# Performance work log

Hardware: AMD Instinct MI355X
Metric: run time of the kernel (lower is better)

Reference implementation:

```python
import jax, jax.numpy as jnp
import numpy as np

B, T, D = 2, 2048, 2048
N_HEADS, N_KV, HEAD_DIM = 16, 8, 128
SOFTCAP = 50.0
BIG_NEG = -2.3819763e38
ROPE_BASE = 10000.0


def apply_rope(x, positions):
    # x: [B, L, N, H], positions: [B, L]
    H = x.shape[-1]
    half = H // 2
    fraction = 2.0 * jnp.arange(half, dtype=jnp.float32) / H
    timescale = ROPE_BASE ** fraction  # [H/2]
    sinusoid = positions.astype(jnp.float32)[:, :, None, None] / timescale[None, None, None, :]  # [B,L,1,H/2]
    sin, cos = jnp.sin(sinusoid), jnp.cos(sinusoid)
    first, second = jnp.split(x, 2, axis=-1)
    out = jnp.concatenate([first * cos - second * sin, second * cos + first * sin], axis=-1)
    return out.astype(x.dtype)


def setup_inputs() -> dict:
    key = jax.random.key(0)
    k1, k2, k3, k4 = jax.random.split(key, 4)
    x = jax.random.normal(k1, (B, T, D), dtype=jnp.float32)
    positions = jnp.broadcast_to(jnp.arange(T, dtype=jnp.int32), (B, T))
    # causal mask [B, 1, T, S]
    attn_mask = jnp.broadcast_to(jnp.tril(jnp.ones((T, T), dtype=bool))[None, None], (B, 1, T, T))
    s = 1.0 / np.sqrt(D)
    w_q = jax.random.normal(k2, (N_HEADS, D, HEAD_DIM), dtype=jnp.float32) * s
    w_kv = jax.random.normal(k3, (2, N_KV, D, HEAD_DIM), dtype=jnp.float32) * s
    w_out = jax.random.normal(k4, (N_HEADS, HEAD_DIM, D), dtype=jnp.float32) * (1.0 / np.sqrt(N_HEADS * HEAD_DIM))
    return {"x": x, "positions": positions, "attn_mask": attn_mask, "w_q": w_q, "w_kv": w_kv, "w_out": w_out}


def reference(x, positions, attn_mask, w_q, w_kv, w_out):
    # projections (GQA branch: num_kv_heads != num_heads)
    q = jnp.einsum('btd,ndh->btnh', x, w_q)            # [B,T,N,H]
    kv = jnp.einsum('bsd,cndh->cbsnh', x, w_kv)        # [2,B,S,K,H]
    k, v = kv[0], kv[1]
    q = apply_rope(q, positions) * (HEAD_DIM ** -0.5)  # rsqrt_head_dim
    k = apply_rope(k, positions)
    G = N_HEADS // N_KV
    q = q.reshape(B, T, N_KV, G, HEAD_DIM)             # B T K G H
    logits = jnp.einsum('btkgh,bskh->bkgts', q, k).astype(jnp.float32)
    logits = jnp.tanh(logits / SOFTCAP) * SOFTCAP
    masked = jnp.where(attn_mask[:, :, None, :, :], logits, BIG_NEG)
    probs = jax.nn.softmax(masked, axis=-1).astype(k.dtype)
    encoded = jnp.einsum('bkgts,bskh->btkgh', probs, v).reshape(B, T, N_HEADS, HEAD_DIM)
    return jnp.einsum('btnh,nhd->btd', encoded, w_out)
```

## Files before the change

kernel.cpp:

```cpp
#include <hip/hip_runtime.h>


typedef unsigned short u16;
typedef __attribute__((ext_vector_type(8))) short short8;
typedef __attribute__((ext_vector_type(4))) float floatx4;

static __device__ __forceinline__ u16 f2b(float f){
  unsigned u = __float_as_uint(f);
  u = (u + 0x7fffu + ((u >> 16) & 1u)) >> 16;
  return (u16)u;
}
static __device__ __forceinline__ float b2f(u16 u){
  return __uint_as_float(((unsigned)u) << 16);
}
static __device__ __forceinline__ void gload16(const u16* g, u16* l){
  __builtin_amdgcn_global_load_lds(
      (const __attribute__((address_space(1))) unsigned int*)g,
      (__attribute__((address_space(3))) unsigned int*)l, 16, 0, 0);
}

static __device__ void tr64(const float* __restrict__ s, u16* __restrict__ d,
                            int sRS, int dRS, float (*t)[65], int tid){
  #pragma unroll
  for(int i = 0; i < 16; i++){
    int idx = tid + 256 * i;
    t[idx >> 6][idx & 63] = s[(long)(idx >> 6) * sRS + (idx & 63)];
  }
  __syncthreads();
  #pragma unroll
  for(int i = 0; i < 16; i++){
    int idx = tid + 256 * i;
    d[(long)(idx >> 6) * dRS + (idx & 63)] = f2b(t[idx & 63][idx >> 6]);
  }
}

__global__ __launch_bounds__(256) void k_prep(
    const float* __restrict__ x, u16* __restrict__ xb,
    const float* __restrict__ wq, u16* __restrict__ wq_t,
    const float* __restrict__ wkv, u16* __restrict__ wkv_t,
    const float* __restrict__ wo, u16* __restrict__ wo_t,
    const int* __restrict__ pos, float* __restrict__ tab){
  __shared__ float t[64][65];
  int blk = blockIdx.x, tid = threadIdx.x;
  if(blk < 8192){
    int i = blk * 256 + tid;
    float4 v = ((const float4*)x)[i];
    ushort4 o = make_ushort4(f2b(v.x), f2b(v.y), f2b(v.z), f2b(v.w));
    ((ushort4*)xb)[i] = o;
  } else if(blk < 9216){
    int q = blk - 8192;
    int bx = q & 1, by = (q >> 1) & 31, bz = q >> 6;
    tr64(wq + (long)bz * 262144 + (long)by * 64 * 128 + bx * 64,
         wq_t + (long)bz * 262144 + (long)bx * 64 * 2048 + by * 64, 128, 2048, t, tid);
  } else if(blk < 10240){
    int q = blk - 9216;
    int bx = q & 1, by = (q >> 1) & 31, bz = q >> 6;
    tr64(wkv + (long)bz * 262144 + (long)by * 64 * 128 + bx * 64,
         wkv_t + (long)bz * 262144 + (long)bx * 64 * 2048 + by * 64, 128, 2048, t, tid);
  } else if(blk < 11264){
    int q = blk - 10240;
    int bx = q & 31, by = q >> 5;
    tr64(wo + (long)by * 64 * 2048 + bx * 64,
         wo_t + (long)bx * 64 * 2048 + by * 64, 2048, 2048, t, tid);
  } else {
    int idx = (blk - 11264) * 256 + tid;
    int row = idx >> 6, h = idx & 63;
    float pf = (float)pos[row];
    float inv = exp2f(-0.20762050593045077f * (float)h);
    float ang = pf * inv;
    tab[(row << 7) + h]      = sinf(ang);
    tab[(row << 7) + 64 + h] = cosf(ang);
  }
}

#define STAGE_A(tt, h) do{ \
  const u16* s_ = Ag + (tt) * 64 + (h) * 262144; \
  u16* d_ = ld + ss * 8192; \
  gload16(s_, d_); gload16(s_ + 131072, d_ + 4096); \
  ss++; if(ss == 10) ss = 0; }while(0)
#define STAGE_B(tt, h) do{ \
  const u16* s_ = Bg + (tt) * 64 + (h) * 262144; \
  u16* d_ = ld + ss * 8192; \
  gload16(s_, d_); gload16(s_ + 131072, d_ + 4096); \
  ss++; if(ss == 10) ss = 0; }while(0)

__global__ __launch_bounds__(512, 2) void k_gemm_qkv(
    const u16* __restrict__ A, const u16* __restrict__ wq_t, const u16* __restrict__ wkv_t,
    const float* __restrict__ tab,
    u16* __restrict__ qb, u16* __restrict__ kb, u16* __restrict__ vtp){
  __shared__ __attribute__((aligned(16))) u16 ring[81920];
  int mt = blockIdx.x, nt = blockIdx.y;
  const u16* Bt = (nt < 8) ? (wq_t + (long)nt * 524288)
                           : (wkv_t + (long)(nt - 8) * 524288);
  int tid = threadIdx.x;
  int lane = tid & 63, wave = tid >> 6, l15 = lane & 15, quad = lane >> 4;
  int wr = wave >> 2, wc = wave & 3;
  int cq0 = quad ^ (l15 & 7), cq1 = cq0 ^ 4;
  int srow = tid >> 3;
  int gch  = (tid & 7) ^ (srow & 7);
  const u16* Ag = A  + ((long)mt * 256 + srow) * 2048 + (gch << 3);
  const u16* Bg = Bt + (long)srow * 2048 + (gch << 3);
  u16* ld = ring + tid * 8;
  int aB = l15 << 6;
  int bB = ((wc & 1) * 64 + l15) << 6;
  int sa = wr;
  int sb = 2 + (wc >> 1);
  int ss = 0;
  floatx4 acc[8][4];
  const floatx4 fz = {0.f, 0.f, 0.f, 0.f};
  #pragma unroll
  for(int m = 0; m < 8; m++)
    #pragma unroll
    for(int n = 0; n < 4; n++) acc[m][n] = fz;

  STAGE_A(0, 0); STAGE_A(0, 1); STAGE_B(0, 0); STAGE_B(0, 1);
  STAGE_A(1, 0); STAGE_A(1, 1);
  asm volatile("s_waitcnt vmcnt(4)" ::: "memory");
  __builtin_amdgcn_s_barrier();

  #pragma unroll 1
  for(int t = 0; t < 32; t++){
    const u16* aS = ring + sa * 8192;
    const u16* bS = ring + sb * 8192;
    int tB = (t < 31) ? t + 1 : 31;
    int tA = (t < 30) ? t + 2 : 31;
    short8 a0[4], a1[4], b0[2], b1[2];
    #pragma unroll
    for(int n = 0; n < 2; n++){
      b0[n] = *(const short8*)(bS + bB + (n << 10) + (cq0 << 3));
      b1[n] = *(const short8*)(bS + bB + (n << 10) + (cq1 << 3));
    }
    #pragma unroll
    for(int m = 0; m < 4; m++){
      a0[m] = *(const short8*)(aS + aB + (m << 10) + (cq0 << 3));
      a1[m] = *(const short8*)(aS + aB + (m << 10) + (cq1 << 3));
    }
    STAGE_B(tB, 0);
    __builtin_amdgcn_s_barrier();
    asm volatile("s_waitcnt lgkmcnt(0)");
    __builtin_amdgcn_s_setprio(1);
    #pragma unroll
    for(int m = 0; m < 4; m++)
      #pragma unroll
      for(int n = 0; n < 2; n++)
        acc[m][n] = __builtin_amdgcn_mfma_f32_16x16x32_bf16(a0[m], b0[n], acc[m][n], 0, 0, 0);
    #pragma unroll
    for(int m = 0; m < 4; m++)
      #pragma unroll
      for(int n = 0; n < 2; n++)
        acc[m][n] = __builtin_amdgcn_mfma_f32_16x16x32_bf16(a1[m], b1[n], acc[m][n], 0, 0, 0);
    __builtin_amdgcn_s_setprio(0);
    __builtin_amdgcn_s_barrier();
    #pragma unroll
    for(int m = 0; m < 4; m++){
      a0[m] = *(const short8*)(aS + aB + 4096 + (m << 10) + (cq0 << 3));
      a1[m] = *(const short8*)(aS + aB + 4096 + (m << 10) + (cq1 << 3));
    }
    STAGE_B(tB, 1);
    __builtin_amdgcn_s_barrier();
    asm volatile("s_waitcnt lgkmcnt(0)");
    __builtin_amdgcn_s_setprio(1);
    #pragma unroll
    for(int m = 0; m < 4; m++)
      #pragma unroll
      for(int n = 0; n < 2; n++)
        acc[4 + m][n] = __builtin_amdgcn_mfma_f32_16x16x32_bf16(a0[m], b0[n], acc[4 + m][n], 0, 0, 0);
    #pragma unroll
    for(int m = 0; m < 4; m++)
      #pragma unroll
      for(int n = 0; n < 2; n++)
        acc[4 + m][n] = __builtin_amdgcn_mfma_f32_16x16x32_bf16(a1[m], b1[n], acc[4 + m][n], 0, 0, 0);
    __builtin_amdgcn_s_setprio(0);
    __builtin_amdgcn_s_barrier();
    #pragma unroll
    for(int n = 0; n < 2; n++){
      b0[n] = *(const short8*)(bS + bB + ((2 + n) << 10) + (cq0 << 3));
      b1[n] = *(const short8*)(bS + bB + ((2 + n) << 10) + (cq1 << 3));
    }
    STAGE_A(tA, 0);
    __builtin_amdgcn_s_barrier();
    asm volatile("s_waitcnt lgkmcnt(0)");
    __builtin_amdgcn_s_setprio(1);
    #pragma unroll
    for(int m = 0; m < 4; m++)
      #pragma unroll
      for(int n = 0; n < 2; n++)
        acc[4 + m][2 + n] = __builtin_amdgcn_mfma_f32_16x16x32_bf16(a0[m], b0[n], acc[4 + m][2 + n], 0, 0, 0);
    #pragma unroll
    for(int m = 0; m < 4; m++)
      #pragma unroll
      for(int n = 0; n < 2; n++)
        acc[4 + m][2 + n] = __builtin_amdgcn_mfma_f32_16x16x32_bf16(a1[m], b1[n], acc[4 + m][2 + n], 0, 0, 0);
    __builtin_amdgcn_s_setprio(0);
    __builtin_amdgcn_s_barrier();
    #pragma unroll
    for(int m = 0; m < 4; m++){
      a0[m] = *(const short8*)(aS + aB + (m << 10) + (cq0 << 3));
      a1[m] = *(const short8*)(aS + aB + (m << 10) + (cq1 << 3));
    }
    STAGE_A(tA, 1);
    asm volatile("s_waitcnt vmcnt(4)" ::: "memory");
    __builtin_amdgcn_s_barrier();
    asm volatile("s_waitcnt lgkmcnt(0)");
    __builtin_amdgcn_s_setprio(1);
    #pragma unroll
    for(int m = 0; m < 4; m++)
      #pragma unroll
      for(int n = 0; n < 2; n++)
        acc[m][2 + n] = __builtin_amdgcn_mfma_f32_16x16x32_bf16(a0[m], b0[n], acc[m][2 + n], 0, 0, 0);
    #pragma unroll
    for(int m = 0; m < 4; m++)
      #pragma unroll
      for(int n = 0; n < 2; n++)
        acc[m][2 + n] = __builtin_amdgcn_mfma_f32_16x16x32_bf16(a1[m], b1[n], acc[m][2 + n], 0, 0, 0);
    __builtin_amdgcn_s_setprio(0);
    __builtin_amdgcn_s_barrier();
    sa += 4; if(sa >= 10) sa -= 10;
    sb += 4; if(sb >= 10) sb -= 10;
  }

  asm volatile("s_waitcnt vmcnt(0)" ::: "memory");
  __syncthreads();
  u16* sT = ring;
  int grow0 = mt * 256;
  int hb = wc >> 1, wcl = wc & 1;
  #pragma unroll 1
  for(int hh = 0; hh < 2; hh++){
    if(hb == hh){
      #pragma unroll
      for(int m = 0; m < 8; m++){
        int row = wr * 128 + m * 16 + quad * 4;
        #pragma unroll
        for(int n = 0; n < 4; n++){
          int colh = wcl * 64 + n * 16 + l15;
          #pragma unroll
          for(int j = 0; j < 4; j++)
            sT[(row + j) * 132 + colh] = f2b(acc[m][n][j]);
        }
      }
    }
    __syncthreads();
    if(nt < 12){
      float scale = (nt < 8) ? 0.08838834764831845f : 1.0f;
      u16* dst = (nt < 8) ? qb : kb;
      int dS   = (nt < 8) ? 2048 : 1024;
      int dcol = (nt < 8) ? (nt * 2 + hh) * 128 : ((nt - 8) * 2 + hh) * 128;
      #pragma unroll
      for(int it = 0; it < 16; it++){
        int idx = tid + 512 * it;
        int row = idx >> 5, cw = idx & 31;
        int grow = grow0 + row;
        unsigned lo = *(const unsigned*)&sT[row * 132 + 2 * cw];
        unsigned hi = *(const unsigned*)&sT[row * 132 + 64 + 2 * cw];
        float2 sn = *(const float2*)&tab[(grow << 7) + 2 * cw];
        float2 cs = *(const float2*)&tab[(grow << 7) + 64 + 2 * cw];
        float x1a = b2f((u16)lo), x1b = b2f((u16)(lo >> 16));
        float x2a = b2f((u16)hi), x2b = b2f((u16)(hi >> 16));
        float o1a = (x1a * cs.x - x2a * sn.x) * scale;
        float o1b = (x1b * cs.y - x2b * sn.y) * scale;
        float o2a = (x2a * cs.x + x1a * sn.x) * scale;
        float o2b = (x2b * cs.y + x1b * sn.y) * scale;
        unsigned w1 = (unsigned)f2b(o1a) | ((unsigned)f2b(o1b) << 16);
        unsigned w2 = (unsigned)f2b(o2a) | ((unsigned)f2b(o2b) << 16);
        *(unsigned*)&dst[(long)grow * dS + dcol + 2 * cw] = w1;
        *(unsigned*)&dst[(long)grow * dS + dcol + 64 + 2 * cw] = w2;
      }
    } else {
      int b = mt >> 3, kvh = (nt - 12) * 2 + hh;
      u16* vt = vtp + (long)(b * 8 + kvh) * 262144;
      int tcol0 = (mt & 7) * 256;
      int h = tid >> 2, s0 = (tid & 3) * 64;
      #pragma unroll
      for(int i = 0; i < 16; i++){
        int s = s0 + i * 4;
        ushort4 v4 = make_ushort4(sT[(s    ) * 132 + h], sT[(s + 1) * 132 + h],
                                  sT[(s + 2) * 132 + h], sT[(s + 3) * 132 + h]);
        *(ushort4*)&vt[(long)h * 2048 + tcol0 + s] = v4;
      }
    }
    __syncthreads();
  }
}
#undef STAGE_A
#undef STAGE_B

__global__ __launch_bounds__(256) void k_gemm_out(
    const u16* __restrict__ A, const u16* __restrict__ Bt0, float* __restrict__ C){
  __shared__ __attribute__((aligned(16))) u16 sA[128 * 64];
  __shared__ __attribute__((aligned(16))) u16 sB[128 * 64];
  int mt = blockIdx.x, nt = blockIdx.y;
  const u16* Bt = Bt0 + (long)nt * 262144;
  int tid = threadIdx.x;
  int lane = tid & 63, wave = tid >> 6, l15 = lane & 15, quad = lane >> 4;
  int ro = (wave & 1) * 64, co = (wave >> 1) * 64;
  int xm7 = l15 & 7;
  int srow = tid >> 3;
  int gch  = (tid & 7) ^ (srow & 7);
  const u16* Ag = A  + ((long)(mt * 128) + srow) * 2048 + (gch << 3);
  const u16* Bg = Bt + (long)srow * 2048 + (gch << 3);
  u16* lA = sA + tid * 8;
  u16* lB = sB + tid * 8;
  floatx4 acc[4][4];
  const floatx4 fz = {0.f, 0.f, 0.f, 0.f};
  #pragma unroll
  for(int r = 0; r < 4; r++)
    #pragma unroll
    for(int c = 0; c < 4; c++) acc[r][c] = fz;
  for(int k0 = 0; k0 < 2048; k0 += 64){
    #pragma unroll
    for(int r = 0; r < 4; r++){
      gload16(Ag + (long)r * 65536 + k0, lA + r * 2048);
      gload16(Bg + (long)r * 65536 + k0, lB + r * 2048);
    }
    __syncthreads();
    #pragma unroll
    for(int ks = 0; ks < 2; ks++){
      short8 af[4], bfr[4];
      #pragma unroll
      for(int r = 0; r < 4; r++)
        af[r]  = *(const short8*)(sA + ((ro + r * 16 + l15) << 6) + ((((ks << 2) | quad) ^ xm7) << 3));
      #pragma unroll
      for(int c = 0; c < 4; c++)
        bfr[c] = *(const short8*)(sB + ((co + c * 16 + l15) << 6) + ((((ks << 2) | quad) ^ xm7) << 3));
      #pragma unroll
      for(int r = 0; r < 4; r++)
        #pragma unroll
        for(int c = 0; c < 4; c++)
          acc[r][c] = __builtin_amdgcn_mfma_f32_16x16x32_bf16(af[r], bfr[c], acc[r][c], 0, 0, 0);
    }
    __syncthreads();
  }
  long rb0 = (long)mt * 128 + ro + quad * 4;
  #pragma unroll
  for(int r = 0; r < 4; r++)
    #pragma unroll
    for(int c = 0; c < 4; c++){
      int col = nt * 128 + co + c * 16 + l15;
      #pragma unroll
      for(int j = 0; j < 4; j++)
        C[(rb0 + r * 16 + j) * 2048 + col] = acc[r][c][j];
    }
}

__global__ __launch_bounds__(256) void k_flash(
    const u16* __restrict__ qb, const u16* __restrict__ kb,
    const u16* __restrict__ vt, u16* __restrict__ enc){
  __shared__ __attribute__((aligned(16))) u16 sK[2 * 64 * 128];
  __shared__ __attribute__((aligned(16))) u16 sVt[2 * 128 * 64];
  __shared__ __attribute__((aligned(16))) u16 sP[4][16][72];
  int qt = 31 - blockIdx.y;
  int hidx = blockIdx.x;
  int b = hidx >> 4, kv = (hidx >> 1) & 7, g = hidx & 1;
  int tid = threadIdx.x;
  int lane = tid & 63, wave = tid >> 6, l15 = lane & 15, quad = lane >> 4;

  short8 qf[4];
  {
    const u16* qg = qb + ((long)b * 2048 + qt * 64 + wave * 16 + l15) * 2048
                       + (kv * 2 + g) * 128 + quad * 8;
    #pragma unroll
    for(int ks = 0; ks < 4; ks++) qf[ks] = *(const short8*)(qg + ks * 32);
  }

  int krow = tid >> 4;
  int kch  = (tid & 15) ^ krow;
  const u16* Kg = kb + ((long)b * 2048 + krow) * 1024 + kv * 128 + (kch << 3);
  int vrow = tid >> 3;
  int vch  = (tid & 7) ^ (vrow & 7);
  const u16* Vg = vt + ((long)(b * 8 + kv) * 128 + vrow) * 2048 + (vch << 3);
  u16* lK = sK  + tid * 8;
  u16* lV = sVt + tid * 8;
  #pragma unroll
  for(int r = 0; r < 4; r++){
    gload16(Kg + (long)r * 16384, lK + r * 2048);
    gload16(Vg + (long)r * 65536, lV + r * 2048);
  }

  float l_loc[4] = {0.f, 0.f, 0.f, 0.f};
  floatx4 o_acc[8];
  const floatx4 fz = {0.f, 0.f, 0.f, 0.f};
  #pragma unroll
  for(int c = 0; c < 8; c++) o_acc[c] = fz;

  const float c1 = 0.057707801635558536f;
  const float c2 = -144.26950408889634f;
  const float c3 = 72.13475204444817f;

  for(int kt = 0; kt <= qt; kt++){
    int buf = (kt & 1) * 8192;
    __syncthreads();
    if(kt < qt){
      int nb = buf ^ 8192;
      #pragma unroll
      for(int r = 0; r < 4; r++){
        gload16(Kg + (long)(kt + 1) * 65536 + (long)r * 16384, lK + nb + r * 2048);
        gload16(Vg + (kt + 1) * 64 + (long)r * 65536, lV + nb + r * 2048);
      }
    }
    floatx4 s_acc[4];
    #pragma unroll
    for(int c = 0; c < 4; c++) s_acc[c] = fz;
    #pragma unroll
    for(int ks = 0; ks < 4; ks++){
      #pragma unroll
      for(int cb = 0; cb < 4; cb++){
        short8 bk = *(const short8*)(sK + buf + ((cb * 16 + l15) << 7)
                                     + ((((ks << 2) | quad) ^ l15) << 3));
        s_acc[cb] = __builtin_amdgcn_mfma_f32_16x16x32_bf16(qf[ks], bk, s_acc[cb], 0, 0, 0);
      }
    }
    if(kt < qt){
      #pragma unroll
      for(int r = 0; r < 4; r++){
        #pragma unroll
        for(int cb = 0; cb < 4; cb++){
          float s = s_acc[cb][r];
          float u = __builtin_amdgcn_exp2f(c1 * s);
          float d = __builtin_amdgcn_rcpf(u + 1.f);
          float p = __builtin_amdgcn_exp2f(__builtin_fmaf(c2, d, c3));
          l_loc[r] += p;
          sP[wave][quad * 4 + r][cb * 16 + l15] = f2b(p);
        }
      }
    } else {
      int rloc = wave * 16 + quad * 4;
      #pragma unroll
      for(int r = 0; r < 4; r++){
        #pragma unroll
        for(int cb = 0; cb < 4; cb++){
          float s = s_acc[cb][r];
          float u = __builtin_amdgcn_exp2f(c1 * s);
          float d = __builtin_amdgcn_rcpf(u + 1.f);
          float p = __builtin_amdgcn_exp2f(__builtin_fmaf(c2, d, c3));
          if(cb * 16 + l15 > rloc + r) p = 0.f;
          l_loc[r] += p;
          sP[wave][quad * 4 + r][cb * 16 + l15] = f2b(p);
        }
      }
    }
    #pragma unroll
    for(int ks2 = 0; ks2 < 2; ks2++){
      short8 ap = *(const short8*)&sP[wave][l15][ks2 * 32 + quad * 8];
      #pragma unroll
      for(int c = 0; c < 8; c++){
        short8 bv = *(const short8*)(sVt + buf + ((c * 16 + l15) << 6)
                                     + ((((ks2 << 2) | quad) ^ (l15 & 7)) << 3));
        o_acc[c] = __builtin_amdgcn_mfma_f32_16x16x32_bf16(ap, bv, o_acc[c], 0, 0, 0);
      }
    }
  }
  #pragma unroll
  for(int r = 0; r < 4; r++){
    float l = l_loc[r];
    #pragma unroll
    for(int off = 1; off < 16; off <<= 1) l += __shfl_xor(l, off);
    float invl = 1.f / l;
    long rowe = (long)b * 2048 + qt * 64 + wave * 16 + quad * 4 + r;
    #pragma unroll
    for(int c = 0; c < 8; c++)
      enc[rowe * 2048 + (kv * 2 + g) * 128 + c * 16 + l15] = f2b(o_acc[c][r] * invl);
  }
}

extern "C" void kernel_launch(void* const* d_in, const int* in_sizes, int n_in,
                              void* d_out, int out_size, void* d_ws, size_t ws_size,
                              hipStream_t stream){
  const float* x     = (const float*)d_in[0];
  const int*   posi  = (const int*)  d_in[1];
  const float* w_q   = (const float*)d_in[3];
  const float* w_kv  = (const float*)d_in[4];
  const float* w_out = (const float*)d_in[5];
  float* out = (float*)d_out;

  char* w = (char*)d_ws;
  u16* xb     = (u16*)(w);
  u16* wq_t   = (u16*)(w + 16777216);
  u16* wkv_t  = (u16*)(w + 25165824);
  u16* wout_t = (u16*)(w + 33554432);
  u16* q_buf  = (u16*)(w + 41943040);
  u16* k_buf  = (u16*)(w + 58720256);
  u16* v_t    = (u16*)(w + 67108864);
  float* tab  = (float*)(w + 75497472);
  u16* enc    = xb;

  k_prep    <<<12288, 256, 0, stream>>>(x, xb, w_q, wq_t, w_kv, wkv_t, w_out, wout_t, posi, tab);
  k_gemm_qkv<<<dim3(16, 16), 512, 0, stream>>>(xb, wq_t, wkv_t, tab, q_buf, k_buf, v_t);
  k_flash   <<<dim3(32, 32), 256, 0, stream>>>(q_buf, k_buf, v_t, enc);
  k_gemm_out<<<dim3(32, 16), 256, 0, stream>>>(enc, wout_t, out);
}
```

Baseline: 323.0 us.

## Split QKV GEMM staging: A via LDS-direct ring, B via register double-buffer

Restructures the QKV projection GEMM pipeline. A tiles now stream into a 12-slot LDS ring through direct-to-LDS loads, staged per quarter. B tiles are loaded into registers one step ahead and written into a double-buffered LDS region. The block-to-tile mapping is also remapped so blocks on the same XCD share A/B tiles for L2 locality. This adds register pressure and extra LDS store traffic, and it relies on a delicate vmcnt accounting that mixes register loads with LDS-direct loads.

Result: no change. 320.8 us (-0.7%).

```diff
diff --git a/kernel.cpp b/kernel.cpp
--- a/kernel.cpp
+++ b/kernel.cpp
@@ -73,23 +73,19 @@
   }
 }
 
-#define STAGE_A(tt, h) do{ \
-  const u16* s_ = Ag + (tt) * 64 + (h) * 262144; \
-  u16* d_ = ld + ss * 8192; \
-  gload16(s_, d_); gload16(s_ + 131072, d_ + 4096); \
-  ss++; if(ss == 10) ss = 0; }while(0)
-#define STAGE_B(tt, h) do{ \
-  const u16* s_ = Bg + (tt) * 64 + (h) * 262144; \
-  u16* d_ = ld + ss * 8192; \
-  gload16(s_, d_); gload16(s_ + 131072, d_ + 4096); \
-  ss++; if(ss == 10) ss = 0; }while(0)
+#define STAGE_AQ(tt, q) do{ \
+  gload16(Ag + (tt) * 64 + (q) * 131072, ldA + ssA * 4096); \
+  ssA++; if(ssA == 12) ssA = 0; }while(0)
 
 __global__ __launch_bounds__(512, 2) void k_gemm_qkv(
     const u16* __restrict__ A, const u16* __restrict__ wq_t, const u16* __restrict__ wkv_t,
     const float* __restrict__ tab,
     u16* __restrict__ qb, u16* __restrict__ kb, u16* __restrict__ vtp){
-  __shared__ __attribute__((aligned(16))) u16 ring[81920];
-  int mt = blockIdx.x, nt = blockIdx.y;
+  __shared__ __attribute__((aligned(16))) u16 lds[81920];
+  int lin = blockIdx.x + (blockIdx.y << 4);
+  int xcd = lin & 7, jj = lin >> 3;
+  int mt = (xcd & 3) * 4 + (jj & 3);
+  int nt = (xcd >> 2) * 8 + (jj >> 2);
   const u16* Bt = (nt < 8) ? (wq_t + (long)nt * 524288)
                            : (wkv_t + (long)(nt - 8) * 524288);
   int tid = threadIdx.x;
@@ -100,12 +96,12 @@
   int gch  = (tid & 7) ^ (srow & 7);
   const u16* Ag = A  + ((long)mt * 256 + srow) * 2048 + (gch << 3);
   const u16* Bg = Bt + (long)srow * 2048 + (gch << 3);
-  u16* ld = ring + tid * 8;
+  u16* bbuf = lds + 49152;
+  u16* ldA = lds + tid * 8;
+  u16* ldB = bbuf + tid * 8;
   int aB = l15 << 6;
-  int bB = ((wc & 1) * 64 + l15) << 6;
-  int sa = wr;
-  int sb = 2 + (wc >> 1);
-  int ss = 0;
+  int sa0 = 2 * wr;
+  int ssA = 0;
   floatx4 acc[8][4];
   const floatx4 fz = {0.f, 0.f, 0.f, 0.f};
   #pragma unroll
@@ -113,29 +109,53 @@
     #pragma unroll
     for(int n = 0; n < 4; n++) acc[m][n] = fz;
 
-  STAGE_A(0, 0); STAGE_A(0, 1); STAGE_B(0, 0); STAGE_B(0, 1);
-  STAGE_A(1, 0); STAGE_A(1, 1);
-  asm volatile("s_waitcnt vmcnt(4)" ::: "memory");
+  short8 bp0 = *(const short8*)(Bg);
+  short8 bp1 = *(const short8*)(Bg + 131072);
+  short8 bp2 = *(const short8*)(Bg + 262144);
+  short8 bp3 = *(const short8*)(Bg + 393216);
+  STAGE_AQ(0, 0); STAGE_AQ(0, 1); STAGE_AQ(0, 2); STAGE_AQ(0, 3);
+  STAGE_AQ(1, 0); STAGE_AQ(1, 1); STAGE_AQ(1, 2); STAGE_AQ(1, 3);
+  short8 bc0 = *(const short8*)(Bg + 64);
+  short8 bc1 = *(const short8*)(Bg + 64 + 131072);
+  short8 bc2 = *(const short8*)(Bg + 64 + 262144);
+  short8 bc3 = *(const short8*)(Bg + 64 + 393216);
+  *(short8*)(ldB)         = bp0;
+  *(short8*)(ldB + 4096)  = bp1;
+  *(short8*)(ldB + 8192)  = bp2;
+  *(short8*)(ldB + 12288) = bp3;
+  asm volatile("s_waitcnt vmcnt(8)" ::: "memory");
+  asm volatile("s_waitcnt lgkmcnt(0)");
   __builtin_amdgcn_s_barrier();
 
   #pragma unroll 1
   for(int t = 0; t < 32; t++){
-    const u16* aS = ring + sa * 8192;
-    const u16* bS = ring + sb * 8192;
-    int tB = (t < 31) ? t + 1 : 31;
+    const u16* aQ0 = lds + sa0 * 4096;
+    const u16* aQ1 = lds + sa0 * 4096 + 4096;
+    const u16* bS  = bbuf + (t & 1) * 16384 + wc * 4096;
     int tA = (t < 30) ? t + 2 : 31;
     short8 a0[4], a1[4], b0[2], b1[2];
+    short8 bn0 = *(const short8*)(Bg + tA * 64);
+    short8 bn1 = *(const short8*)(Bg + tA * 64 + 131072);
+    short8 bn2 = *(const short8*)(Bg + tA * 64 + 262144);
+    short8 bn3 = *(const short8*)(Bg + tA * 64 + 393216);
+    {
+      u16* bw = ldB + ((t + 1) & 1) * 16384;
+      *(short8*)(bw)         = bc0;
+      *(short8*)(bw + 4096)  = bc1;
+      *(short8*)(bw + 8192)  = bc2;
+      *(short8*)(bw + 12288) = bc3;
+    }
     #pragma unroll
     for(int n = 0; n < 2; n++){
-      b0[n] = *(const short8*)(bS + bB + (n << 10) + (cq0 << 3));
-      b1[n] = *(const short8*)(bS + bB + (n << 10) + (cq1 << 3));
+      b0[n] = *(const short8*)(bS + aB + (n << 10) + (cq0 << 3));
+      b1[n] = *(const short8*)(bS + aB + (n << 10) + (cq1 << 3));
     }
     #pragma unroll
     for(int m = 0; m < 4; m++){
-      a0[m] = *(const short8*)(aS + aB + (m << 10) + (cq0 << 3));
-      a1[m] = *(const short8*)(aS + aB + (m << 10) + (cq1 << 3));
-    }
-    STAGE_B(tB, 0);
+      a0[m] = *(const short8*)(aQ0 + aB + (m << 10) + (cq0 << 3));
+      a1[m] = *(const short8*)(aQ0 + aB + (m << 10) + (cq1 << 3));
+    }
+    STAGE_AQ(tA, 0);
     __builtin_amdgcn_s_barrier();
     asm volatile("s_waitcnt lgkmcnt(0)");
     __builtin_amdgcn_s_setprio(1);
@@ -153,10 +173,10 @@
     __builtin_amdgcn_s_barrier();
     #pragma unroll
     for(int m = 0; m < 4; m++){
-      a0[m] = *(const short8*)(aS + aB + 4096 + (m << 10) + (cq0 << 3));
-      a1[m] = *(const short8*)(aS + aB + 4096 + (m << 10) + (cq1 << 3));
-    }
-    STAGE_B(tB, 1);
+      a0[m] = *(const short8*)(aQ1 + aB + (m << 10) + (cq0 << 3));
+      a1[m] = *(const short8*)(aQ1 + aB + (m << 10) + (cq1 << 3));
+    }
+    STAGE_AQ(tA, 1);
     __builtin_amdgcn_s_barrier();
     asm volatile("s_waitcnt lgkmcnt(0)");
     __builtin_amdgcn_s_setprio(1);
@@ -174,10 +194,10 @@
     __builtin_amdgcn_s_barrier();
     #pragma unroll
     for(int n = 0; n < 2; n++){
-      b0[n] = *(const short8*)(bS + bB + ((2 + n) << 10) + (cq0 << 3));
-      b1[n] = *(const short8*)(bS + bB + ((2 + n) << 10) + (cq1 << 3));
-    }
-    STAGE_A(tA, 0);
+      b0[n] = *(const short8*)(bS + aB + ((2 + n) << 10) + (cq0 << 3));
+      b1[n] = *(const short8*)(bS + aB + ((2 + n) << 10) + (cq1 << 3));
+    }
+    STAGE_AQ(tA, 2);
     __builtin_amdgcn_s_barrier();
     asm volatile("s_waitcnt lgkmcnt(0)");
     __builtin_amdgcn_s_setprio(1);
@@ -195,11 +215,11 @@
     __builtin_amdgcn_s_barrier();
     #pragma unroll
     for(int m = 0; m < 4; m++){
-      a0[m] = *(const short8*)(aS + aB + (m << 10) + (cq0 << 3));
-      a1[m] = *(const short8*)(aS + aB + (m << 10) + (cq1 << 3));
-    }
-    STAGE_A(tA, 1);
-    asm volatile("s_waitcnt vmcnt(4)" ::: "memory");
+      a0[m] = *(const short8*)(aQ0 + aB + (m << 10) + (cq0 << 3));
+      a1[m] = *(const short8*)(aQ0 + aB + (m << 10) + (cq1 << 3));
+    }
+    STAGE_AQ(tA, 3);
+    asm volatile("s_waitcnt vmcnt(8)" ::: "memory");
     __builtin_amdgcn_s_barrier();
     asm volatile("s_waitcnt lgkmcnt(0)");
     __builtin_amdgcn_s_setprio(1);
@@ -215,13 +235,13 @@
         acc[m][2 + n] = __builtin_amdgcn_mfma_f32_16x16x32_bf16(a1[m], b1[n], acc[m][2 + n], 0, 0, 0);
     __builtin_amdgcn_s_setprio(0);
     __builtin_amdgcn_s_barrier();
-    sa += 4; if(sa >= 10) sa -= 10;
-    sb += 4; if(sb >= 10) sb -= 10;
+    bc0 = bn0; bc1 = bn1; bc2 = bn2; bc3 = bn3;
+    sa0 += 4; if(sa0 >= 12) sa0 -= 12;
   }
 
   asm volatile("s_waitcnt vmcnt(0)" ::: "memory");
   __syncthreads();
-  u16* sT = ring;
+  u16* sT = lds;
   int grow0 = mt * 256;
   int hb = wc >> 1, wcl = wc & 1;
   #pragma unroll 1
@@ -281,8 +301,7 @@
     __syncthreads();
   }
 }
-#undef STAGE_A
-#undef STAGE_B
+#undef STAGE_AQ
 
 __global__ __launch_bounds__(256) void k_gemm_out(
     const u16* __restrict__ A, const u16* __restrict__ Bt0, float* __restrict__ C){
```

## Keep A fragments in registers across phases and remap blocks to XCDs

Applied to the files above, without the earlier changes.

The QKV GEMM main loop keeps both halves of the A-tile fragments in separate register arrays. This removes the fourth LDS reload of A and merges the last two MFMA phases, cutting barriers per K step from four rounds to three. Stage issues are rebalanced (both B halves staged together). Block indices are also remapped so blocks on the same XCD share M/N tiles for better L2 reuse. The cost is higher VGPR pressure, which could cause spills at 2 blocks per CU, plus changed load/wait timing.

Measured after the change: 311.9 us. 1.04x faster.

```diff
diff --git a/kernel.cpp b/kernel.cpp
--- a/kernel.cpp
+++ b/kernel.cpp
@@ -89,7 +89,10 @@
     const float* __restrict__ tab,
     u16* __restrict__ qb, u16* __restrict__ kb, u16* __restrict__ vtp){
   __shared__ __attribute__((aligned(16))) u16 ring[81920];
-  int mt = blockIdx.x, nt = blockIdx.y;
+  int lin = blockIdx.x + (blockIdx.y << 4);
+  int xcd = lin & 7, jj = lin >> 3;
+  int mt = (xcd & 3) * 4 + (jj & 3);
+  int nt = (xcd >> 2) * 8 + (jj >> 2);
   const u16* Bt = (nt < 8) ? (wq_t + (long)nt * 524288)
                            : (wkv_t + (long)(nt - 8) * 524288);
   int tid = threadIdx.x;
@@ -124,7 +127,7 @@
     const u16* bS = ring + sb * 8192;
     int tB = (t < 31) ? t + 1 : 31;
     int tA = (t < 30) ? t + 2 : 31;
-    short8 a0[4], a1[4], b0[2], b1[2];
+    short8 am0k0[4], am0k1[4], am1k0[4], am1k1[4], b0[2], b1[2];
     #pragma unroll
     for(int n = 0; n < 2; n++){
       b0[n] = *(const short8*)(bS + bB + (n << 10) + (cq0 << 3));
@@ -132,10 +135,10 @@
     }
     #pragma unroll
     for(int m = 0; m < 4; m++){
-      a0[m] = *(const short8*)(aS + aB + (m << 10) + (cq0 << 3));
-      a1[m] = *(const short8*)(aS + aB + (m << 10) + (cq1 << 3));
-    }
-    STAGE_B(tB, 0);
+      am0k0[m] = *(const short8*)(aS + aB + (m << 10) + (cq0 << 3));
+      am0k1[m] = *(const short8*)(aS + aB + (m << 10) + (cq1 << 3));
+    }
+    STAGE_B(tB, 0); STAGE_B(tB, 1);
     __builtin_amdgcn_s_barrier();
     asm volatile("s_waitcnt lgkmcnt(0)");
     __builtin_amdgcn_s_setprio(1);
@@ -143,20 +146,20 @@
     for(int m = 0; m < 4; m++)
       #pragma unroll
       for(int n = 0; n < 2; n++)
-        acc[m][n] = __builtin_amdgcn_mfma_f32_16x16x32_bf16(a0[m], b0[n], acc[m][n], 0, 0, 0);
-    #pragma unroll
-    for(int m = 0; m < 4; m++)
-      #pragma unroll
-      for(int n = 0; n < 2; n++)
-        acc[m][n] = __builtin_amdgcn_mfma_f32_16x16x32_bf16(a1[m], b1[n], acc[m][n], 0, 0, 0);
+        acc[m][n] = __builtin_amdgcn_mfma_f32_16x16x32_bf16(am0k0[m], b0[n], acc[m][n], 0, 0, 0);
+    #pragma unroll
+    for(int m = 0; m < 4; m++)
+      #pragma unroll
+      for(int n = 0; n < 2; n++)
+        acc[m][n] = __builtin_amdgcn_mfma_f32_16x16x32_bf16(am0k1[m], b1[n], acc[m][n], 0, 0, 0);
     __builtin_amdgcn_s_setprio(0);
     __builtin_amdgcn_s_barrier();
     #pragma unroll
     for(int m = 0; m < 4; m++){
-      a0[m] = *(const short8*)(aS + aB + 4096 + (m << 10) + (cq0 << 3));
-      a1[m] = *(const short8*)(aS + aB + 4096 + (m << 10) + (cq1 << 3));
-    }
-    STAGE_B(tB, 1);
+      am1k0[m] = *(const short8*)(aS + aB + 4096 + (m << 10) + (cq0 << 3));
+      am1k1[m] = *(const short8*)(aS + aB + 4096 + (m << 10) + (cq1 << 3));
+    }
+    STAGE_A(tA, 0);
     __builtin_amdgcn_s_barrier();
     asm volatile("s_waitcnt lgkmcnt(0)");
     __builtin_amdgcn_s_setprio(1);
@@ -164,12 +167,12 @@
     for(int m = 0; m < 4; m++)
       #pragma unroll
       for(int n = 0; n < 2; n++)
-        acc[4 + m][n] = __builtin_amdgcn_mfma_f32_16x16x32_bf16(a0[m], b0[n], acc[4 + m][n], 0, 0, 0);
-    #pragma unroll
-    for(int m = 0; m < 4; m++)
-      #pragma unroll
-      for(int n = 0; n < 2; n++)
-        acc[4 + m][n] = __builtin_amdgcn_mfma_f32_16x16x32_bf16(a1[m], b1[n], acc[4 + m][n], 0, 0, 0);
+        acc[4 + m][n] = __builtin_amdgcn_mfma_f32_16x16x32_bf16(am1k0[m], b0[n], acc[4 + m][n], 0, 0, 0);
+    #pragma unroll
+    for(int m = 0; m < 4; m++)
+      #pragma unroll
+      for(int n = 0; n < 2; n++)
+        acc[4 + m][n] = __builtin_amdgcn_mfma_f32_16x16x32_bf16(am1k1[m], b1[n], acc[4 + m][n], 0, 0, 0);
     __builtin_amdgcn_s_setprio(0);
     __builtin_amdgcn_s_barrier();
     #pragma unroll
@@ -177,7 +180,8 @@
       b0[n] = *(const short8*)(bS + bB + ((2 + n) << 10) + (cq0 << 3));
       b1[n] = *(const short8*)(bS + bB + ((2 + n) << 10) + (cq1 << 3));
     }
-    STAGE_A(tA, 0);
+    STAGE_A(tA, 1);
+    asm volatile("s_waitcnt vmcnt(4)" ::: "memory");
     __builtin_amdgcn_s_barrier();
     asm volatile("s_waitcnt lgkmcnt(0)");
     __builtin_amdgcn_s_setprio(1);
@@ -185,34 +189,22 @@
     for(int m = 0; m < 4; m++)
       #pragma unroll
       for(int n = 0; n < 2; n++)
-        acc[4 + m][2 + n] = __builtin_amdgcn_mfma_f32_16x16x32_bf16(a0[m], b0[n], acc[4 + m][2 + n], 0, 0, 0);
-    #pragma unroll
-    for(int m = 0; m < 4; m++)
-      #pragma unroll
-      for(int n = 0; n < 2; n++)
-        acc[4 + m][2 + n] = __builtin_amdgcn_mfma_f32_16x16x32_bf16(a1[m], b1[n], acc[4 + m][2 + n], 0, 0, 0);
-    __builtin_amdgcn_s_setprio(0);
-    __builtin_amdgcn_s_barrier();
-    #pragma unroll
-    for(int m = 0; m < 4; m++){
-      a0[m] = *(const short8*)(aS + aB + (m << 10) + (cq0 << 3));
-      a1[m] = *(const short8*)(aS + aB + (m << 10) + (cq1 << 3));
-    }
-    STAGE_A(tA, 1);
-    asm volatile("s_waitcnt vmcnt(4)" ::: "memory");
-    __builtin_amdgcn_s_barrier();
-    asm volatile("s_waitcnt lgkmcnt(0)");
-    __builtin_amdgcn_s_setprio(1);
-    #pragma unroll
-    for(int m = 0; m < 4; m++)
-      #pragma unroll
-      for(int n = 0; n < 2; n++)
-        acc[m][2 + n] = __builtin_amdgcn_mfma_f32_16x16x32_bf16(a0[m], b0[n], acc[m][2 + n], 0, 0, 0);
-    #pragma unroll
-    for(int m = 0; m < 4; m++)
-      #pragma unroll
-      for(int n = 0; n < 2; n++)
-        acc[m][2 + n] = __builtin_amdgcn_mfma_f32_16x16x32_bf16(a1[m], b1[n], acc[m][2 + n], 0, 0, 0);
+        acc[4 + m][2 + n] = __builtin_amdgcn_mfma_f32_16x16x32_bf16(am1k0[m], b0[n], acc[4 + m][2 + n], 0, 0, 0);
+    #pragma unroll
+    for(int m = 0; m < 4; m++)
+      #pragma unroll
+      for(int n = 0; n < 2; n++)
+        acc[4 + m][2 + n] = __builtin_amdgcn_mfma_f32_16x16x32_bf16(am1k1[m], b1[n], acc[4 + m][2 + n], 0, 0, 0);
+    #pragma unroll
+    for(int m = 0; m < 4; m++)
+      #pragma unroll
+      for(int n = 0; n < 2; n++)
+        acc[m][2 + n] = __builtin_amdgcn_mfma_f32_16x16x32_bf16(am0k0[m], b0[n], acc[m][2 + n], 0, 0, 0);
+    #pragma unroll
+    for(int m = 0; m < 4; m++)
+      #pragma unroll
+      for(int n = 0; n < 2; n++)
+        acc[m][2 + n] = __builtin_amdgcn_mfma_f32_16x16x32_bf16(am0k1[m], b1[n], acc[m][2 + n], 0, 0, 0);
     __builtin_amdgcn_s_setprio(0);
     __builtin_amdgcn_s_barrier();
     sa += 4; if(sa >= 10) sa -= 10;
```
